# Optimization experiments

Measured on AMD Instinct MI355X. Metric: run time of the kernel, lower is better.

## Reference

```python
import jax, jax.numpy as jnp
import numpy as np

D_MODEL = 1024
NUM_HEADS = 16
HEAD_DIM = D_MODEL // NUM_HEADS
BATCH = 4
SEQ = 2048


def setup_inputs() -> dict:
    key = jax.random.key(0)
    k_x, k_wqkv, k_bqkv, k_wo, k_bo = jax.random.split(key, 5)
    x = jax.random.normal(k_x, (BATCH, SEQ, D_MODEL), dtype=jnp.float32)
    # Linear params (flax Linear stores kernel as [in, out])
    s1 = 1.0 / np.sqrt(D_MODEL)
    W_qkv = jax.random.normal(k_wqkv, (D_MODEL, 3 * D_MODEL), dtype=jnp.float32) * s1
    b_qkv = jax.random.normal(k_bqkv, (3 * D_MODEL,), dtype=jnp.float32) * 0.01
    W_out = jax.random.normal(k_wo, (D_MODEL, D_MODEL), dtype=jnp.float32) * s1
    b_out = jax.random.normal(k_bo, (D_MODEL,), dtype=jnp.float32) * 0.01
    return {"x": x, "W_qkv": W_qkv, "b_qkv": b_qkv, "W_out": W_out, "b_out": b_out}


def reference(x, W_qkv, b_qkv, W_out, b_out):
    B, S, _ = x.shape
    qkv = x @ W_qkv + b_qkv                                   # [B,S,3D]
    qkv = qkv.reshape(B, S, 3, NUM_HEADS, HEAD_DIM)
    q, k, v = jnp.split(qkv, 3, axis=2)
    q = q.squeeze(2).transpose(0, 2, 1, 3)                    # [B,H,S,d]
    k = k.squeeze(2).transpose(0, 2, 1, 3)
    v = v.squeeze(2).transpose(0, 2, 1, 3)
    scores = jnp.einsum('bhqd,bhkd->bhqk', q, k) / jnp.sqrt(jnp.float32(HEAD_DIM))
    causal = jnp.tril(jnp.ones((S, S), dtype=bool))[None, None]
    scores = jnp.where(causal, scores, jnp.float32(-1e10))
    attn = jax.nn.softmax(scores, axis=-1)                    # [B,H,S,S]
    out = jnp.einsum('bhqk,bhkd->bhqd', attn, v)              # [B,H,S,d]
    out = out.transpose(0, 2, 1, 3).reshape(B, S, D_MODEL)
    return out @ W_out + b_out
```

## Files before the change

kernel.cpp:

```cpp
#include <hip/hip_runtime.h>

#define SEQ 2048
#define DM 1024
#define NH 16
#define HD 64
#define BATCH 4
#define M_TOK (BATCH * SEQ)

typedef _Float16 f16;
typedef _Float16 f16x8 __attribute__((ext_vector_type(8)));
typedef float f32x4 __attribute__((ext_vector_type(4)));

__device__ __forceinline__ f32x4 mfma16(f16x8 a, f16x8 b, f32x4 c) {
  return __builtin_amdgcn_mfma_f32_16x16x32_f16(a, b, c, 0, 0, 0);
}

__device__ __forceinline__ void gload16(const void* g, void* l) {
  __builtin_amdgcn_global_load_lds((const __attribute__((address_space(1))) void*)g,
                                   (__attribute__((address_space(3))) void*)l, 16, 0, 0);
}

__global__ void cvt_f16_kernel(const float* __restrict__ in, f16* __restrict__ out, int n8) {
  int i = blockIdx.x * blockDim.x + threadIdx.x;
  if (i >= n8) return;
  float4 a = ((const float4*)in)[2 * i];
  float4 b = ((const float4*)in)[2 * i + 1];
  f16x8 v;
  v[0] = (f16)a.x; v[1] = (f16)a.y; v[2] = (f16)a.z; v[3] = (f16)a.w;
  v[4] = (f16)b.x; v[5] = (f16)b.y; v[6] = (f16)b.z; v[7] = (f16)b.w;
  *(f16x8*)(out + 8 * i) = v;
}

__global__ void transpose_cvt_kernel(const float* __restrict__ W, f16* __restrict__ Wt,
                                     int K, int N) {
  __shared__ float t[32][33];
  int tx = threadIdx.x & 31, ty = threadIdx.x >> 5;
  int c0 = blockIdx.x * 32, r0 = blockIdx.y * 32;
#pragma unroll
  for (int i = 0; i < 4; ++i)
    t[ty + 8 * i][tx] = W[(r0 + ty + 8 * i) * N + c0 + tx];
  __syncthreads();
#pragma unroll
  for (int i = 0; i < 4; ++i)
    Wt[(c0 + ty + 8 * i) * K + r0 + tx] = (f16)t[tx][ty + 8 * i];
}

template <typename OutT, bool SPLIT_V>
__global__ __launch_bounds__(256) void gemm_tn(const f16* __restrict__ A,
                                               const f16* __restrict__ Bt,
                                               const float* __restrict__ bias,
                                               OutT* __restrict__ C, f16* __restrict__ Vt,
                                               int M, int N, int K, int ldc) {
  __shared__ f16 Alds[128 * 64];
  __shared__ f16 Blds[128 * 64];
  const int tid = threadIdx.x;
  const int lane = tid & 63, wid = tid >> 6;
  const int l15 = lane & 15, l4 = lane >> 4;
  const int m0 = blockIdx.y * 128, n0 = blockIdx.x * 128;
  const int wr = wid >> 1, wc = wid & 1;

  f32x4 acc[4][4] = {};

  for (int k0 = 0; k0 < K; k0 += 64) {
    __syncthreads();
#pragma unroll
    for (int i = 0; i < 4; ++i) {
      int c = (wid * 4 + i) * 64 + lane;
      int row = c >> 3, cb = (c & 7) << 4;
      int sw = cb ^ ((row & 7) << 4);
      const char* gA = (const char*)(A + ((size_t)(m0 + row) * K + k0)) + sw;
      gload16(gA, (char*)Alds + ((wid * 4 + i) << 10));
      const char* gB = (const char*)(Bt + ((size_t)(n0 + row) * K + k0)) + sw;
      gload16(gB, (char*)Blds + ((wid * 4 + i) << 10));
    }
    asm volatile("s_waitcnt vmcnt(0)" ::: "memory");
    __syncthreads();

#pragma unroll
    for (int ks = 0; ks < 2; ++ks) {
      f16x8 af[4], bf[4];
      int cb = ((ks * 4 + l4) << 4);
#pragma unroll
      for (int mi = 0; mi < 4; ++mi) {
        int row = wr * 64 + mi * 16 + l15;
        af[mi] = *(const f16x8*)((const char*)Alds + row * 128 + (cb ^ ((row & 7) << 4)));
      }
#pragma unroll
      for (int ni = 0; ni < 4; ++ni) {
        int row = wc * 64 + ni * 16 + l15;
        bf[ni] = *(const f16x8*)((const char*)Blds + row * 128 + (cb ^ ((row & 7) << 4)));
      }
#pragma unroll
      for (int mi = 0; mi < 4; ++mi)
#pragma unroll
        for (int ni = 0; ni < 4; ++ni)
          acc[mi][ni] = mfma16(af[mi], bf[ni], acc[mi][ni]);
    }
  }

#pragma unroll
  for (int ni = 0; ni < 4; ++ni) {
    int col = n0 + wc * 64 + ni * 16 + l15;
    float bv = bias[col];
#pragma unroll
    for (int mi = 0; mi < 4; ++mi)
#pragma unroll
      for (int r = 0; r < 4; ++r) {
        int rowg = m0 + wr * 64 + mi * 16 + l4 * 4 + r;
        float val = acc[mi][ni][r] + bv;
        if (SPLIT_V && col >= 2 * DM) {
          int hdv = col - 2 * DM;
          int b = rowg >> 11, s = rowg & (SEQ - 1);
          Vt[(size_t)(b * 1024 + hdv) * SEQ + s] = (f16)val;
        } else {
          C[(size_t)rowg * ldc + col] = (OutT)val;
        }
      }
  }
}

__global__ __launch_bounds__(256) void attn_kernel(const f16* __restrict__ qkh,
                                                   const f16* __restrict__ vtg,
                                                   f16* __restrict__ outp) {
  __shared__ f16 Klds[2][64 * 64];
  __shared__ f16 Vlds[2][64 * 64];
  __shared__ f16 Plds[4][16 * 64];
  const int tid = threadIdx.x;
  const int lane = tid & 63, wid = tid >> 6;
  const int l15 = lane & 15, l4 = lane >> 4;
  const int blk = blockIdx.x;
  const int swz = (blk & 7) * 256 + (blk >> 3);
  const int bh = swz >> 5;
  const int b = bh >> 4, h = bh & 15;
  const int q0 = (31 - (swz & 31)) << 6;

  const int qrow = q0 + wid * 16 + l15;
  const f16* qp = qkh + (size_t)(b * SEQ + qrow) * 2048 + h * HD;
  const f16x8 qf0 = *(const f16x8*)(qp + l4 * 8);
  const f16x8 qf1 = *(const f16x8*)(qp + 32 + l4 * 8);

  const char* kbase = (const char*)qkh + ((size_t)(b * SEQ) * 2048 + 1024 + h * HD) * 2;
  const char* vbase = (const char*)vtg + ((size_t)(bh * 64) * SEQ) * 2;
  int srow[2], ssw[2], schunk[2];
#pragma unroll
  for (int i = 0; i < 2; ++i) {
    int c = (wid * 2 + i) * 64 + lane;
    srow[i] = c >> 3;
    int cb = (c & 7) << 4;
    ssw[i] = cb ^ ((srow[i] & 7) << 4);
    schunk[i] = (wid * 2 + i) << 10;
  }

  f32x4 o[4] = {};
  float m_run[4], l_run[4];
#pragma unroll
  for (int r = 0; r < 4; ++r) { m_run[r] = -3.0e38f; l_run[r] = 0.f; }

  f16x8 onef;
#pragma unroll
  for (int e = 0; e < 8; ++e) onef[e] = (f16)1.0f;

  const int ntile = (q0 >> 6) + 1;

#pragma unroll
  for (int i = 0; i < 2; ++i) {
    gload16(kbase + (size_t)srow[i] * 4096 + ssw[i], (char*)Klds[0] + schunk[i]);
    gload16(vbase + (size_t)srow[i] * 4096 + ssw[i], (char*)Vlds[0] + schunk[i]);
  }
  __syncthreads();

  for (int t = 0; t < ntile; ++t) {
    const int cur = t & 1;
    const int kt = t << 6;
    if (t + 1 < ntile) {
      const int kn = kt + 64;
#pragma unroll
      for (int i = 0; i < 2; ++i) {
        gload16(kbase + (size_t)(kn + srow[i]) * 4096 + ssw[i], (char*)Klds[cur ^ 1] + schunk[i]);
        gload16(vbase + (size_t)srow[i] * 4096 + kn * 2 + ssw[i], (char*)Vlds[cur ^ 1] + schunk[i]);
      }
    }

    f32x4 p4[4];
#pragma unroll
    for (int nt = 0; nt < 4; ++nt) {
      f32x4 s = {};
#pragma unroll
      for (int c = 0; c < 2; ++c) {
        int row = nt * 16 + l15;
        int cb = ((c * 4 + l4) << 4);
        f16x8 kf = *(const f16x8*)((const char*)Klds[cur] + row * 128 + (cb ^ ((row & 7) << 4)));
        s = mfma16(c == 0 ? qf0 : qf1, kf, s);
      }
#pragma unroll
      for (int r = 0; r < 4; ++r) {
        int q = q0 + wid * 16 + l4 * 4 + r;
        int k = kt + nt * 16 + l15;
        s[r] = (k <= q) ? s[r] * 0.125f : -3.0e38f;
      }
      p4[nt] = s;
    }

    float mx[4];
#pragma unroll
    for (int r = 0; r < 4; ++r)
      mx[r] = fmaxf(fmaxf(p4[0][r], p4[1][r]), fmaxf(p4[2][r], p4[3][r]));
#pragma unroll
    for (int off = 1; off < 16; off <<= 1)
#pragma unroll
      for (int r = 0; r < 4; ++r)
        mx[r] = fmaxf(mx[r], __shfl_xor(mx[r], off, 64));

    float alpha[4];
#pragma unroll
    for (int r = 0; r < 4; ++r) {
      float mn = fmaxf(m_run[r], mx[r]);
      alpha[r] = exp2f((m_run[r] - mn) * 1.44269504f);
      m_run[r] = mn;
    }
#pragma unroll
    for (int nt = 0; nt < 4; ++nt)
#pragma unroll
      for (int r = 0; r < 4; ++r) {
        float p = exp2f((p4[nt][r] - m_run[r]) * 1.44269504f);
        int row = l4 * 4 + r;
        int cb = (nt * 16 + l15) * 2;
        *(f16*)((char*)Plds[wid] + row * 128 + (cb ^ ((row & 7) << 4))) = (f16)p;
      }
#pragma unroll
    for (int tt = 0; tt < 4; ++tt)
#pragma unroll
      for (int r = 0; r < 4; ++r)
        o[tt][r] *= alpha[r];

    f32x4 accl = {};
#pragma unroll
    for (int c = 0; c < 2; ++c) {
      int cb = ((c * 4 + l4) << 4);
      int prow = l15;
      f16x8 pf = *(const f16x8*)((const char*)Plds[wid] + prow * 128 + (cb ^ ((prow & 7) << 4)));
#pragma unroll
      for (int tt = 0; tt < 4; ++tt) {
        int row = tt * 16 + l15;
        f16x8 vf = *(const f16x8*)((const char*)Vlds[cur] + row * 128 + (cb ^ ((row & 7) << 4)));
        o[tt] = mfma16(pf, vf, o[tt]);
      }
      accl = mfma16(pf, onef, accl);
    }
#pragma unroll
    for (int r = 0; r < 4; ++r)
      l_run[r] = l_run[r] * alpha[r] + accl[r];

    __syncthreads();
  }

#pragma unroll
  for (int tt = 0; tt < 4; ++tt)
#pragma unroll
    for (int r = 0; r < 4; ++r) {
      int q = q0 + wid * 16 + l4 * 4 + r;
      int dv = tt * 16 + l15;
      outp[(size_t)(b * SEQ + q) * DM + h * HD + dv] = (f16)(o[tt][r] / l_run[r]);
    }
}

extern "C" void kernel_launch(void* const* d_in, const int* in_sizes, int n_in,
                              void* d_out, int out_size, void* d_ws, size_t ws_size,
                              hipStream_t stream) {
  const float* x = (const float*)d_in[0];
  const float* Wqkv = (const float*)d_in[1];
  const float* bqkv = (const float*)d_in[2];
  const float* Wout = (const float*)d_in[3];
  const float* bout = (const float*)d_in[4];
  float* out = (float*)d_out;

  char* ws = (char*)d_ws;
  f16* xh = (f16*)(ws);
  f16* qkh = (f16*)(ws + 16777216);
  f16* vt = (f16*)(ws + 16777216 + 33554432);
  f16* wqkvT = (f16*)(ws + 16777216 + 33554432 + 16777216);
  f16* woutT = (f16*)(ws + 16777216 + 33554432 + 16777216 + 6291456);
  f16* attno = xh;

  cvt_f16_kernel<<<(M_TOK * DM / 8 + 255) / 256, 256, 0, stream>>>(x, xh, M_TOK * DM / 8);
  transpose_cvt_kernel<<<dim3(3 * DM / 32, DM / 32), 256, 0, stream>>>(Wqkv, wqkvT, DM, 3 * DM);
  transpose_cvt_kernel<<<dim3(DM / 32, DM / 32), 256, 0, stream>>>(Wout, woutT, DM, DM);
  gemm_tn<f16, true><<<dim3(3 * DM / 128, M_TOK / 128), 256, 0, stream>>>(
      xh, wqkvT, bqkv, qkh, vt, M_TOK, 3 * DM, DM, 2048);
  attn_kernel<<<BATCH * NH * (SEQ / 64), 256, 0, stream>>>(qkh, vt, attno);
  gemm_tn<float, false><<<dim3(DM / 128, M_TOK / 128), 256, 0, stream>>>(
      attno, woutT, bout, out, nullptr, M_TOK, DM, DM, DM);
}
```

Baseline: 369.7 us.

## Rewrite attention with 32x32 MFMA, 128-query blocks and register-resident P

The attention kernel now processes 128 queries per block with 32 queries per wave, using 32x32x16 MFMA to compute S^T = K·Q^T, so each lane owns one query row. P stays in registers and is rearranged with cross-half shuffles instead of a round-trip through LDS. The row sum is done with plain adds rather than an extra MFMA against ones. The Q scaling is folded into the Q fragments in f16, the rescale of O is skipped when no row max rises, and masking is limited to the diagonal tile. The launch is halved, which raises per-block work and register pressure, and waves above the diagonal sit idle during the extra tile.

Measured after the change: 342.3 us. -7.4%, faster.

```diff
diff --git a/kernel.cpp b/kernel.cpp
--- a/kernel.cpp
+++ b/kernel.cpp
@@ -9,10 +9,15 @@
 
 typedef _Float16 f16;
 typedef _Float16 f16x8 __attribute__((ext_vector_type(8)));
+typedef _Float16 f16x4 __attribute__((ext_vector_type(4)));
 typedef float f32x4 __attribute__((ext_vector_type(4)));
+typedef float f32x16 __attribute__((ext_vector_type(16)));
 
 __device__ __forceinline__ f32x4 mfma16(f16x8 a, f16x8 b, f32x4 c) {
   return __builtin_amdgcn_mfma_f32_16x16x32_f16(a, b, c, 0, 0, 0);
+}
+__device__ __forceinline__ f32x16 mfma32(f16x8 a, f16x8 b, f32x16 c) {
+  return __builtin_amdgcn_mfma_f32_32x32x16_f16(a, b, c, 0, 0, 0);
 }
 
 __device__ __forceinline__ void gload16(const void* g, void* l) {
@@ -119,25 +124,32 @@
   }
 }
 
+union H2u { struct { f16 lo, hi; } s; unsigned u; };
+union F8u { f16x8 v; unsigned u[4]; };
+
 __global__ __launch_bounds__(256) void attn_kernel(const f16* __restrict__ qkh,
                                                    const f16* __restrict__ vtg,
                                                    f16* __restrict__ outp) {
   __shared__ f16 Klds[2][64 * 64];
   __shared__ f16 Vlds[2][64 * 64];
-  __shared__ f16 Plds[4][16 * 64];
   const int tid = threadIdx.x;
   const int lane = tid & 63, wid = tid >> 6;
-  const int l15 = lane & 15, l4 = lane >> 4;
+  const int lq = lane & 31, hi = lane >> 5;
   const int blk = blockIdx.x;
-  const int swz = (blk & 7) * 256 + (blk >> 3);
-  const int bh = swz >> 5;
+  const int swz = (blk & 7) * 128 + (blk >> 3);
+  const int bh = swz >> 4;
   const int b = bh >> 4, h = bh & 15;
-  const int q0 = (31 - (swz & 31)) << 6;
-
-  const int qrow = q0 + wid * 16 + l15;
-  const f16* qp = qkh + (size_t)(b * SEQ + qrow) * 2048 + h * HD;
-  const f16x8 qf0 = *(const f16x8*)(qp + l4 * 8);
-  const f16x8 qf1 = *(const f16x8*)(qp + 32 + l4 * 8);
+  const int q0 = (15 - (swz & 15)) << 7;
+  const int q0w = q0 + wid * 32;
+  const int q_g = q0w + lq;
+
+  const f16* qp = qkh + (size_t)(b * SEQ + q_g) * 2048 + h * HD;
+  f16x8 qf[4];
+#pragma unroll
+  for (int s = 0; s < 4; ++s) {
+    qf[s] = *(const f16x8*)(qp + s * 16 + hi * 8);
+    qf[s] = qf[s] * (f16)0.125f;
+  }
 
   const char* kbase = (const char*)qkh + ((size_t)(b * SEQ) * 2048 + 1024 + h * HD) * 2;
   const char* vbase = (const char*)vtg + ((size_t)(bh * 64) * SEQ) * 2;
@@ -146,21 +158,15 @@
   for (int i = 0; i < 2; ++i) {
     int c = (wid * 2 + i) * 64 + lane;
     srow[i] = c >> 3;
-    int cb = (c & 7) << 4;
-    ssw[i] = cb ^ ((srow[i] & 7) << 4);
+    ssw[i] = ((c & 7) << 4) ^ ((srow[i] & 7) << 4);
     schunk[i] = (wid * 2 + i) << 10;
   }
 
-  f32x4 o[4] = {};
-  float m_run[4], l_run[4];
-#pragma unroll
-  for (int r = 0; r < 4; ++r) { m_run[r] = -3.0e38f; l_run[r] = 0.f; }
-
-  f16x8 onef;
-#pragma unroll
-  for (int e = 0; e < 8; ++e) onef[e] = (f16)1.0f;
-
-  const int ntile = (q0 >> 6) + 1;
+  f32x16 o0 = {}, o1 = {};
+  float m_run = -3.0e38f, l_run = 0.f;
+  const int ntile = (q0 >> 6) + 2;
+  const int ntw = (q0w >> 6) + 1;
+  const float L2E = 1.44269504f;
 
 #pragma unroll
   for (int i = 0; i < 2; ++i) {
@@ -181,87 +187,92 @@
       }
     }
 
-    f32x4 p4[4];
-#pragma unroll
-    for (int nt = 0; nt < 4; ++nt) {
-      f32x4 s = {};
-#pragma unroll
-      for (int c = 0; c < 2; ++c) {
-        int row = nt * 16 + l15;
-        int cb = ((c * 4 + l4) << 4);
-        f16x8 kf = *(const f16x8*)((const char*)Klds[cur] + row * 128 + (cb ^ ((row & 7) << 4)));
-        s = mfma16(c == 0 ? qf0 : qf1, kf, s);
-      }
-#pragma unroll
-      for (int r = 0; r < 4; ++r) {
-        int q = q0 + wid * 16 + l4 * 4 + r;
-        int k = kt + nt * 16 + l15;
-        s[r] = (k <= q) ? s[r] * 0.125f : -3.0e38f;
-      }
-      p4[nt] = s;
-    }
-
-    float mx[4];
-#pragma unroll
-    for (int r = 0; r < 4; ++r)
-      mx[r] = fmaxf(fmaxf(p4[0][r], p4[1][r]), fmaxf(p4[2][r], p4[3][r]));
-#pragma unroll
-    for (int off = 1; off < 16; off <<= 1)
-#pragma unroll
-      for (int r = 0; r < 4; ++r)
-        mx[r] = fmaxf(mx[r], __shfl_xor(mx[r], off, 64));
-
-    float alpha[4];
-#pragma unroll
-    for (int r = 0; r < 4; ++r) {
-      float mn = fmaxf(m_run[r], mx[r]);
-      alpha[r] = exp2f((m_run[r] - mn) * 1.44269504f);
-      m_run[r] = mn;
-    }
-#pragma unroll
-    for (int nt = 0; nt < 4; ++nt)
-#pragma unroll
-      for (int r = 0; r < 4; ++r) {
-        float p = exp2f((p4[nt][r] - m_run[r]) * 1.44269504f);
-        int row = l4 * 4 + r;
-        int cb = (nt * 16 + l15) * 2;
-        *(f16*)((char*)Plds[wid] + row * 128 + (cb ^ ((row & 7) << 4))) = (f16)p;
-      }
-#pragma unroll
-    for (int tt = 0; tt < 4; ++tt)
-#pragma unroll
-      for (int r = 0; r < 4; ++r)
-        o[tt][r] *= alpha[r];
-
-    f32x4 accl = {};
-#pragma unroll
-    for (int c = 0; c < 2; ++c) {
-      int cb = ((c * 4 + l4) << 4);
-      int prow = l15;
-      f16x8 pf = *(const f16x8*)((const char*)Plds[wid] + prow * 128 + (cb ^ ((prow & 7) << 4)));
-#pragma unroll
-      for (int tt = 0; tt < 4; ++tt) {
-        int row = tt * 16 + l15;
-        f16x8 vf = *(const f16x8*)((const char*)Vlds[cur] + row * 128 + (cb ^ ((row & 7) << 4)));
-        o[tt] = mfma16(pf, vf, o[tt]);
-      }
-      accl = mfma16(pf, onef, accl);
-    }
-#pragma unroll
-    for (int r = 0; r < 4; ++r)
-      l_run[r] = l_run[r] * alpha[r] + accl[r];
-
+    if (t < ntw) {
+      f32x16 st0 = {}, st1 = {};
+#pragma unroll
+      for (int s = 0; s < 4; ++s) {
+        int cb = ((2 * s + hi) << 4);
+        f16x8 kf0 = *(const f16x8*)((const char*)Klds[cur] + lq * 128 + (cb ^ ((lq & 7) << 4)));
+        f16x8 kf1 =
+            *(const f16x8*)((const char*)Klds[cur] + (32 + lq) * 128 + (cb ^ ((lq & 7) << 4)));
+        st0 = mfma32(kf0, qf[s], st0);
+        st1 = mfma32(kf1, qf[s], st1);
+      }
+      if (t == ntw - 1) {
+#pragma unroll
+        for (int r = 0; r < 16; ++r) {
+          int kl = (r & 3) + 8 * (r >> 2) + 4 * hi;
+          if (kt + kl > q_g) st0[r] = -3.0e38f;
+          if (kt + 32 + kl > q_g) st1[r] = -3.0e38f;
+        }
+      }
+      float mx = st0[0];
+#pragma unroll
+      for (int r = 1; r < 16; ++r) mx = fmaxf(mx, st0[r]);
+#pragma unroll
+      for (int r = 0; r < 16; ++r) mx = fmaxf(mx, st1[r]);
+      mx = fmaxf(mx, __shfl_xor(mx, 32));
+      if (__any(mx > m_run)) {
+        float mn = fmaxf(m_run, mx);
+        float al = exp2f((m_run - mn) * L2E);
+        m_run = mn;
+        l_run *= al;
+        o0 = o0 * al;
+        o1 = o1 * al;
+      }
+      const float negmL = -m_run * L2E;
+#pragma unroll
+      for (int r = 0; r < 16; ++r) st0[r] = exp2f(fmaf(st0[r], L2E, negmL));
+#pragma unroll
+      for (int r = 0; r < 16; ++r) st1[r] = exp2f(fmaf(st1[r], L2E, negmL));
+      float sm = st0[0];
+#pragma unroll
+      for (int r = 1; r < 16; ++r) sm += st0[r];
+#pragma unroll
+      for (int r = 0; r < 16; ++r) sm += st1[r];
+      sm += __shfl_xor(sm, 32);
+      l_run += sm;
+
+#pragma unroll
+      for (int s = 0; s < 4; ++s) {
+        const f32x16& ps = (s < 2) ? st0 : st1;
+        const int r0 = 8 * (s & 1);
+        H2u a0, a1, a2, a3;
+        a0.s.lo = (f16)ps[r0 + 0]; a0.s.hi = (f16)ps[r0 + 1];
+        a1.s.lo = (f16)ps[r0 + 2]; a1.s.hi = (f16)ps[r0 + 3];
+        a2.s.lo = (f16)ps[r0 + 4]; a2.s.hi = (f16)ps[r0 + 5];
+        a3.s.lo = (f16)ps[r0 + 6]; a3.s.hi = (f16)ps[r0 + 7];
+        unsigned ux = __shfl_xor(a0.u, 32), vx = __shfl_xor(a1.u, 32);
+        unsigned wx = __shfl_xor(a2.u, 32), zx = __shfl_xor(a3.u, 32);
+        F8u pb;
+        pb.u[0] = hi ? wx : a0.u;
+        pb.u[1] = hi ? zx : a1.u;
+        pb.u[2] = hi ? a2.u : ux;
+        pb.u[3] = hi ? a3.u : vx;
+        int vb = ((2 * s + hi) << 4);
+        f16x8 vf0 = *(const f16x8*)((const char*)Vlds[cur] + lq * 128 + (vb ^ ((lq & 7) << 4)));
+        f16x8 vf1 =
+            *(const f16x8*)((const char*)Vlds[cur] + (32 + lq) * 128 + (vb ^ ((lq & 7) << 4)));
+        o0 = mfma32(vf0, pb.v, o0);
+        o1 = mfma32(vf1, pb.v, o1);
+      }
+    }
     __syncthreads();
   }
 
-#pragma unroll
-  for (int tt = 0; tt < 4; ++tt)
-#pragma unroll
-    for (int r = 0; r < 4; ++r) {
-      int q = q0 + wid * 16 + l4 * 4 + r;
-      int dv = tt * 16 + l15;
-      outp[(size_t)(b * SEQ + q) * DM + h * HD + dv] = (f16)(o[tt][r] / l_run[r]);
-    }
+  float rl = 1.0f / l_run;
+  f16* outb = outp + (size_t)(b * SEQ + q_g) * DM + h * HD;
+#pragma unroll
+  for (int dvt = 0; dvt < 2; ++dvt) {
+    const f32x16& ov = dvt ? o1 : o0;
+#pragma unroll
+    for (int rg = 0; rg < 4; ++rg) {
+      f16x4 w4;
+#pragma unroll
+      for (int j = 0; j < 4; ++j) w4[j] = (f16)(ov[rg * 4 + j] * rl);
+      *(f16x4*)(outb + dvt * 32 + 8 * rg + 4 * hi) = w4;
+    }
+  }
 }
 
 extern "C" void kernel_launch(void* const* d_in, const int* in_sizes, int n_in,
@@ -287,7 +298,7 @@
   transpose_cvt_kernel<<<dim3(DM / 32, DM / 32), 256, 0, stream>>>(Wout, woutT, DM, DM);
   gemm_tn<f16, true><<<dim3(3 * DM / 128, M_TOK / 128), 256, 0, stream>>>(
       xh, wqkvT, bqkv, qkh, vt, M_TOK, 3 * DM, DM, 2048);
-  attn_kernel<<<BATCH * NH * (SEQ / 64), 256, 0, stream>>>(qkh, vt, attno);
+  attn_kernel<<<BATCH * NH * (SEQ / 128), 256, 0, stream>>>(qkh, vt, attno);
   gemm_tn<float, false><<<dim3(DM / 128, M_TOK / 128), 256, 0, stream>>>(
       attno, woutT, bout, out, nullptr, M_TOK, DM, DM, DM);
 }
```
